# Kernel tuning notes

Measured on AMD Instinct MI355X. Metric: run time of the kernel, lower is better.

## Reference

```python
import jax, jax.numpy as jnp
import numpy as np

T = 256   # time steps
F = 64    # features per step
H = 32    # LSTM hidden size
FORGET_BIAS = 1.0  # TF LSTMCell default


def setup_inputs() -> dict:
    key = jax.random.key(0)
    k1, k2, k3 = jax.random.split(key, 3)
    B = 16384
    x = jax.random.normal(k1, (B, T * F), dtype=jnp.float32)
    W_lstm = jax.random.normal(k2, (F + H, 4 * H), dtype=jnp.float32) * 0.1
    b_lstm = jnp.zeros((4 * H,), dtype=jnp.float32)
    W_dense = jax.random.normal(k3, (H, 1), dtype=jnp.float32) * 0.1
    b_dense = jnp.zeros((1,), dtype=jnp.float32)
    return {"x": x, "W_lstm": W_lstm, "b_lstm": b_lstm,
            "W_dense": W_dense, "b_dense": b_dense}


def reference(x, W_lstm, b_lstm, W_dense, b_dense):
    B = x.shape[0]
    # [B, T*F] -> [T, B, F] for scan over time
    xs = x.reshape(B, T, F).transpose(1, 0, 2)

    def step(carry, x_t):
        c, h = carry
        # TF LSTMCell: concat([inputs, h]) @ kernel + bias, gate order i, j, f, o
        gates = jnp.concatenate([x_t, h], axis=-1) @ W_lstm + b_lstm
        i, j, f, o = jnp.split(gates, 4, axis=-1)
        c_new = c * jax.nn.sigmoid(f + FORGET_BIAS) + jax.nn.sigmoid(i) * jnp.tanh(j)
        h_new = jnp.tanh(c_new) * jax.nn.sigmoid(o)
        return (c_new, h_new), None

    c0 = jnp.zeros((B, H), dtype=x.dtype)
    h0 = jnp.zeros((B, H), dtype=x.dtype)
    (c_T, h_T), _ = jax.lax.scan(step, (c0, h0), xs)

    # dense(1) + ELU on the final hidden state, then flatten like predict()
    out = jax.nn.elu(h_T @ W_dense + b_dense)
    return out.reshape(-1)
```

## Files before the change

kernel.cpp:

```cpp
#include <hip/hip_runtime.h>
#include <stdint.h>

#define T_STEPS 256
#define F_IN 64
#define L2E 1.44269504f

typedef __bf16 bf16x8 __attribute__((ext_vector_type(8)));
typedef float f32x4 __attribute__((ext_vector_type(4)));
typedef uint32_t u32;
typedef uint32_t u32x2 __attribute__((ext_vector_type(2)));
typedef uint32_t u32x4 __attribute__((ext_vector_type(4)));

#define GLDS16(gp, lp)                                                         \
    __builtin_amdgcn_global_load_lds(                                          \
        (const __attribute__((address_space(1))) unsigned int*)(gp),           \
        (__attribute__((address_space(3))) unsigned int*)(lp), 16, 0, 0)

static __device__ __forceinline__ u32 pk2(float lo, float hi) {
    unsigned short a = __builtin_bit_cast(unsigned short, (__bf16)lo);
    unsigned short b = __builtin_bit_cast(unsigned short, (__bf16)hi);
    return (u32)a | ((u32)b << 16);
}

__global__ __launch_bounds__(128, 2)
void lstm_fused(const float* __restrict__ x,
                const float* __restrict__ Wl,
                const float* __restrict__ bl,
                const float* __restrict__ Wd,
                const float* __restrict__ bd,
                float* __restrict__ out)
{
    __shared__ __align__(16) float  xs[4][1024];
    __shared__ __align__(16) __bf16 hf[2][64][8];

    const int lane = threadIdx.x & 63;
    const int wid  = threadIdx.x >> 6;
    const int cl   = lane & 15;
    const int g4   = lane >> 4;
    const int rowBase = blockIdx.x * 16;

    bf16x8 wfrag[3][4];
#pragma unroll
    for (int kc = 0; kc < 3; ++kc) {
#pragma unroll
        for (int qi = 0; qi < 4; ++qi) {
            bf16x8 v;
#pragma unroll
            for (int j = 0; j < 8; ++j)
                v[j] = (__bf16)Wl[(kc * 32 + g4 * 8 + j) * 128 + (2 * qi + wid) * 16 + cl];
            wfrag[kc][qi] = v;
        }
    }

    float KI[4], KJ[4], KF[4], KO[4];
    {
        const int u0 = wid * 16 + g4 * 4;
#pragma unroll
        for (int r = 0; r < 4; ++r) {
            KI[r] = -L2E        *  bl[      u0 + r];
            KJ[r] = -2.0f * L2E *  bl[ 32 + u0 + r];
            KF[r] = -L2E        * (bl[ 64 + u0 + r] + 1.0f);
            KO[r] = -L2E        *  bl[ 96 + u0 + r];
        }
    }
    const float bd0 = bd[0];
    const f32x4 wdA = *(const f32x4*)(Wd + g4 * 8);
    const f32x4 wdB = *(const f32x4*)(Wd + g4 * 8 + 4);

    const float* gbase = x + (size_t)(rowBase + (lane >> 2)) * (size_t)(T_STEPS * F_IN)
                           + (size_t)(((lane & 3) ^ ((lane >> 3) & 3)) * 4);

    if (threadIdx.x < 64)
        *reinterpret_cast<u32x4*>(&hf[0][threadIdx.x][0]) = u32x4{0u, 0u, 0u, 0u};

    asm volatile("s_waitcnt vmcnt(0)" ::: "memory");
    __builtin_amdgcn_sched_barrier(0);

#pragma unroll
    for (int s = 0; s < 3; ++s) {
        const float* gp = gbase + s * F_IN + wid * 32;
        GLDS16(gp,      &xs[s][wid * 512]);
        GLDS16(gp + 16, &xs[s][wid * 512 + 256]);
    }

    asm volatile("s_waitcnt vmcnt(4) lgkmcnt(0)" ::: "memory");
    __builtin_amdgcn_sched_barrier(0);
    __builtin_amdgcn_s_barrier();
    __builtin_amdgcn_sched_barrier(0);

    const int swz = (cl >> 1) & 3;
    const int c0  = ((g4 & 1) * 2)     ^ swz;
    const int c1  = ((g4 & 1) * 2 + 1) ^ swz;
    const int kA  = (g4 >> 1) * 256 + cl * 16;
    const int kB  = kA + 512;
    const f32x4 z4 = {0.f, 0.f, 0.f, 0.f};

    const int tT = (2 * wid + (g4 >> 1)) * 16 + cl;
    const int e0 = (g4 & 1) * 4;

    float c_st[4] = {0.f, 0.f, 0.f, 0.f};

#define STEP(TT, SLOT) do {                                                    \
    const int par = (SLOT) & 1;                                                \
     \
    const float* sl = &xs[SLOT][0];                                            \
    f32x4 xr0 = *(const f32x4*)(sl + kA + c0 * 4);                             \
    f32x4 xr1 = *(const f32x4*)(sl + kA + c1 * 4);                             \
    f32x4 xr2 = *(const f32x4*)(sl + kB + c0 * 4);                             \
    f32x4 xr3 = *(const f32x4*)(sl + kB + c1 * 4);                             \
    bf16x8 ah = *reinterpret_cast<const bf16x8*>(&hf[par][lane][0]);           \
                                                   \
    const int tpf = ((TT) + 3 < T_STEPS) ? (TT) + 3 : T_STEPS - 1;             \
    const float* gp = gbase + tpf * F_IN + wid * 32;                           \
    GLDS16(gp,      &xs[((SLOT)+3)&3][wid * 512]);                             \
    GLDS16(gp + 16, &xs[((SLOT)+3)&3][wid * 512 + 256]);                       \
    bf16x8 ax0, ax1;                                                           \
    _Pragma("unroll")                                                          \
    for (int j = 0; j < 4; ++j) {                                              \
        ax0[j]     = (__bf16)xr0[j];                                           \
        ax0[4 + j] = (__bf16)xr1[j];                                           \
        ax1[j]     = (__bf16)xr2[j];                                           \
        ax1[4 + j] = (__bf16)xr3[j];                                           \
    }                                                                          \
    f32x4 acc[4];                                                              \
    __builtin_amdgcn_s_setprio(1);                                             \
    _Pragma("unroll")                                                          \
    for (int qi = 0; qi < 4; ++qi) {                                           \
        f32x4 a = __builtin_amdgcn_mfma_f32_16x16x32_bf16(wfrag[0][qi], ax0, z4, 0, 0, 0); \
        a = __builtin_amdgcn_mfma_f32_16x16x32_bf16(wfrag[1][qi], ax1, a, 0, 0, 0);        \
        a = __builtin_amdgcn_mfma_f32_16x16x32_bf16(wfrag[2][qi], ah,  a, 0, 0, 0);        \
        acc[qi] = a;                                                           \
    }                                                                          \
    __builtin_amdgcn_s_setprio(0);                                             \
    \
    float hh[4];                                                               \
    _Pragma("unroll")                                                          \
    for (int r = 0; r < 4; ++r) {                                              \
        float I  = __builtin_amdgcn_exp2f(__builtin_fmaf(acc[0][r], -L2E,        KI[r])); \
        float J  = __builtin_amdgcn_exp2f(__builtin_fmaf(acc[1][r], -2.0f * L2E, KJ[r])); \
        float P  = (1.0f - J) * __builtin_amdgcn_rcpf((1.0f + I) * (1.0f + J)); \
        float Fv = __builtin_amdgcn_exp2f(__builtin_fmaf(acc[2][r], -L2E,        KF[r])); \
        float S  = __builtin_amdgcn_rcpf(1.0f + Fv);                           \
        float cn = __builtin_fmaf(c_st[r], S, P);                              \
        float C  = __builtin_amdgcn_exp2f(-2.0f * L2E * cn);                   \
        float O  = __builtin_amdgcn_exp2f(__builtin_fmaf(acc[3][r], -L2E,      KO[r])); \
        hh[r] = (1.0f - C) * __builtin_amdgcn_rcpf((1.0f + C) * (1.0f + O));   \
        c_st[r] = cn;                                                          \
    }                                                                          \
    *reinterpret_cast<u32x2*>(&hf[par ^ 1][tT][e0]) =                          \
        u32x2{pk2(hh[0], hh[1]), pk2(hh[2], hh[3])};                           \
    asm volatile("s_waitcnt vmcnt(4) lgkmcnt(0)" ::: "memory");                \
    __builtin_amdgcn_sched_barrier(0);                                         \
    __builtin_amdgcn_s_barrier();                                              \
    __builtin_amdgcn_sched_barrier(0);                                         \
} while (0)

    for (int t = 0; t < T_STEPS; t += 4) {
        STEP(t,     0);
        STEP(t + 1, 1);
        STEP(t + 2, 2);
        STEP(t + 3, 3);
    }
#undef STEP

    if (wid == 0) {
        bf16x8 hfin = *reinterpret_cast<const bf16x8*>(&hf[0][lane][0]);
        float v = 0.f;
#pragma unroll
        for (int j = 0; j < 4; ++j) {
            v = __builtin_fmaf((float)hfin[j],     wdA[j], v);
            v = __builtin_fmaf((float)hfin[4 + j], wdB[j], v);
        }
        v += __shfl_xor(v, 16, 64);
        v += __shfl_xor(v, 32, 64);
        if (lane < 16) {
            float z = v + bd0;
            out[rowBase + lane] = z > 0.f ? z : (__expf(z) - 1.0f);
        }
    }
}

extern "C" void kernel_launch(void* const* d_in, const int* in_sizes, int n_in,
                              void* d_out, int out_size, void* d_ws, size_t ws_size,
                              hipStream_t stream) {
    const float* x  = (const float*)d_in[0];
    const float* Wl = (const float*)d_in[1];
    const float* bl = (const float*)d_in[2];
    const float* Wd = (const float*)d_in[3];
    const float* bd = (const float*)d_in[4];
    float* out = (float*)d_out;

    const int rows = out_size;
    const int grid = (rows + 15) / 16;
    hipLaunchKernelGGL(lstm_fused, dim3(grid), dim3(128), 0, stream,
                       x, Wl, bl, Wd, bd, out);
}
```

Before: 262.3 us.

## Batch x prefetch into 4-step stages with 8-slot LDS ring

Replaces per-step prefetch of one timestep into a 4-slot LDS ring with a batched prefetch of four timesteps every fourth step into an 8-slot ring. Each wave now loads whole 64-float rows for two timesteps instead of half rows for every step. The vmcnt wait is now needed only once per four steps, which removes per-step memory waits from the serial recurrence. In exchange LDS use doubles, which may reduce occupancy, and each issue burst is larger.

New measurement: 262.9 us. Within noise of the previous version (+0.2%).

```diff
diff --git a/kernel.cpp b/kernel.cpp
--- a/kernel.cpp
+++ b/kernel.cpp
@@ -30,7 +30,7 @@
                 const float* __restrict__ bd,
                 float* __restrict__ out)
 {
-    __shared__ __align__(16) float  xs[4][1024];
+    __shared__ __align__(16) float  xs[8][1024];
     __shared__ __align__(16) __bf16 hf[2][64][8];
 
     const int lane = threadIdx.x & 63;
@@ -76,14 +76,22 @@
     asm volatile("s_waitcnt vmcnt(0)" ::: "memory");
     __builtin_amdgcn_sched_barrier(0);
 
-#pragma unroll
-    for (int s = 0; s < 3; ++s) {
-        const float* gp = gbase + s * F_IN + wid * 32;
-        GLDS16(gp,      &xs[s][wid * 512]);
-        GLDS16(gp + 16, &xs[s][wid * 512 + 256]);
-    }
-
-    asm volatile("s_waitcnt vmcnt(4) lgkmcnt(0)" ::: "memory");
+#define STAGE(TB) do {                                                         \
+    _Pragma("unroll")                                                          \
+    for (int s2 = 0; s2 < 2; ++s2) {                                           \
+        const int st  = (TB) + 2 * wid + s2;                                   \
+        const int sl8 = st & 7;                                                \
+        const float* gp = gbase + st * F_IN;                                   \
+        GLDS16(gp,      &xs[sl8][0]);                                          \
+        GLDS16(gp + 16, &xs[sl8][256]);                                        \
+        GLDS16(gp + 32, &xs[sl8][512]);                                        \
+        GLDS16(gp + 48, &xs[sl8][768]);                                        \
+    }                                                                          \
+} while (0)
+
+    STAGE(0);
+    STAGE(4);
+    asm volatile("s_waitcnt vmcnt(8) lgkmcnt(0)" ::: "memory");
     __builtin_amdgcn_sched_barrier(0);
     __builtin_amdgcn_s_barrier();
     __builtin_amdgcn_sched_barrier(0);
@@ -100,20 +108,14 @@
 
     float c_st[4] = {0.f, 0.f, 0.f, 0.f};
 
-#define STEP(TT, SLOT) do {                                                    \
-    const int par = (SLOT) & 1;                                                \
-     \
-    const float* sl = &xs[SLOT][0];                                            \
+#define STEP(TT, PH) do {                                                      \
+    const int par = (TT) & 1;                                                  \
+    const float* sl = &xs[(TT) & 7][0];                                        \
     f32x4 xr0 = *(const f32x4*)(sl + kA + c0 * 4);                             \
     f32x4 xr1 = *(const f32x4*)(sl + kA + c1 * 4);                             \
     f32x4 xr2 = *(const f32x4*)(sl + kB + c0 * 4);                             \
     f32x4 xr3 = *(const f32x4*)(sl + kB + c1 * 4);                             \
     bf16x8 ah = *reinterpret_cast<const bf16x8*>(&hf[par][lane][0]);           \
-                                                   \
-    const int tpf = ((TT) + 3 < T_STEPS) ? (TT) + 3 : T_STEPS - 1;             \
-    const float* gp = gbase + tpf * F_IN + wid * 32;                           \
-    GLDS16(gp,      &xs[((SLOT)+3)&3][wid * 512]);                             \
-    GLDS16(gp + 16, &xs[((SLOT)+3)&3][wid * 512 + 256]);                       \
     bf16x8 ax0, ax1;                                                           \
     _Pragma("unroll")                                                          \
     for (int j = 0; j < 4; ++j) {                                              \
@@ -132,7 +134,6 @@
         acc[qi] = a;                                                           \
     }                                                                          \
     __builtin_amdgcn_s_setprio(0);                                             \
-    \
     float hh[4];                                                               \
     _Pragma("unroll")                                                          \
     for (int r = 0; r < 4; ++r) {                                              \
@@ -149,7 +150,16 @@
     }                                                                          \
     *reinterpret_cast<u32x2*>(&hf[par ^ 1][tT][e0]) =                          \
         u32x2{pk2(hh[0], hh[1]), pk2(hh[2], hh[3])};                           \
-    asm volatile("s_waitcnt vmcnt(4) lgkmcnt(0)" ::: "memory");                \
+    if ((PH) == 3) {                                                           \
+        if ((TT) + 5 < T_STEPS) {                                              \
+            STAGE((TT) + 5);                                                   \
+            asm volatile("s_waitcnt vmcnt(8) lgkmcnt(0)" ::: "memory");        \
+        } else {                                                               \
+            asm volatile("s_waitcnt vmcnt(0) lgkmcnt(0)" ::: "memory");        \
+        }                                                                      \
+    } else {                                                                   \
+        asm volatile("s_waitcnt lgkmcnt(0)" ::: "memory");                     \
+    }                                                                          \
     __builtin_amdgcn_sched_barrier(0);                                         \
     __builtin_amdgcn_s_barrier();                                              \
     __builtin_amdgcn_sched_barrier(0);                                         \
@@ -162,6 +172,7 @@
         STEP(t + 3, 3);
     }
 #undef STEP
+#undef STAGE
 
     if (wid == 0) {
         bf16x8 hfin = *reinterpret_cast<const bf16x8*>(&hf[0][lane][0]);
```

## Give each wave independent rows with two interleaved row groups, removing block barriers

Applied to the files above, without the earlier changes.

Instead of two waves splitting the gate columns of one 16-row tile and syncing through shared memory every step, each wave now owns 32 rows (two 16-row groups) and computes all 128 gate columns itself. This removes the per-step s_barrier, and the two independent recurrences are interleaved to hide MFMA and transcendental latency. Prefetch moves to a 3-slot per-wave ring staged two steps ahead. In exchange each wave keeps twice the weight fragments in registers, launch bounds drop to one block per SIMD pair, and the grid shrinks to a quarter as many blocks, so fewer waves may be resident to hide memory latency.

Result: slower. 401.9 us (+53.2%).

```diff
diff --git a/kernel.cpp b/kernel.cpp
--- a/kernel.cpp
+++ b/kernel.cpp
@@ -22,7 +22,7 @@
     return (u32)a | ((u32)b << 16);
 }
 
-__global__ __launch_bounds__(128, 2)
+__global__ __launch_bounds__(128, 1)
 void lstm_fused(const float* __restrict__ x,
                 const float* __restrict__ Wl,
                 const float* __restrict__ bl,
@@ -30,63 +30,69 @@
                 const float* __restrict__ bd,
                 float* __restrict__ out)
 {
-    __shared__ __align__(16) float  xs[4][1024];
-    __shared__ __align__(16) __bf16 hf[2][64][8];
+    __shared__ __align__(16) float  xs[2][3][2][1024];
+    __shared__ __align__(16) __bf16 hb[2][2][16][32];
 
     const int lane = threadIdx.x & 63;
     const int wid  = threadIdx.x >> 6;
     const int cl   = lane & 15;
     const int g4   = lane >> 4;
-    const int rowBase = blockIdx.x * 16;
-
-    bf16x8 wfrag[3][4];
+    const int rowBase = blockIdx.x * 64 + wid * 32;
+
+    bf16x8 wfrag[3][8];
 #pragma unroll
     for (int kc = 0; kc < 3; ++kc) {
 #pragma unroll
-        for (int qi = 0; qi < 4; ++qi) {
+        for (int qi = 0; qi < 8; ++qi) {
             bf16x8 v;
 #pragma unroll
             for (int j = 0; j < 8; ++j)
-                v[j] = (__bf16)Wl[(kc * 32 + g4 * 8 + j) * 128 + (2 * qi + wid) * 16 + cl];
+                v[j] = (__bf16)Wl[(kc * 32 + g4 * 8 + j) * 128 + qi * 16 + cl];
             wfrag[kc][qi] = v;
         }
     }
 
-    float KI[4], KJ[4], KF[4], KO[4];
-    {
-        const int u0 = wid * 16 + g4 * 4;
+    float KI[2][4], KJ[2][4], KF[2][4], KO[2][4];
+#pragma unroll
+    for (int uh = 0; uh < 2; ++uh) {
+        const int u0 = uh * 16 + g4 * 4;
 #pragma unroll
         for (int r = 0; r < 4; ++r) {
-            KI[r] = -L2E        *  bl[      u0 + r];
-            KJ[r] = -2.0f * L2E *  bl[ 32 + u0 + r];
-            KF[r] = -L2E        * (bl[ 64 + u0 + r] + 1.0f);
-            KO[r] = -L2E        *  bl[ 96 + u0 + r];
+            KI[uh][r] = -L2E        *  bl[      u0 + r];
+            KJ[uh][r] = -2.0f * L2E *  bl[ 32 + u0 + r];
+            KF[uh][r] = -L2E        * (bl[ 64 + u0 + r] + 1.0f);
+            KO[uh][r] = -L2E        *  bl[ 96 + u0 + r];
         }
     }
     const float bd0 = bd[0];
-    const f32x4 wdA = *(const f32x4*)(Wd + g4 * 8);
-    const f32x4 wdB = *(const f32x4*)(Wd + g4 * 8 + 4);
-
-    const float* gbase = x + (size_t)(rowBase + (lane >> 2)) * (size_t)(T_STEPS * F_IN)
-                           + (size_t)(((lane & 3) ^ ((lane >> 3) & 3)) * 4);
-
-    if (threadIdx.x < 64)
-        *reinterpret_cast<u32x4*>(&hf[0][threadIdx.x][0]) = u32x4{0u, 0u, 0u, 0u};
+    const f32x4 wd0 = *(const f32x4*)(Wd + g4 * 8);
+    const f32x4 wd1 = *(const f32x4*)(Wd + g4 * 8 + 4);
+
+    const float* gbA = x + (size_t)(rowBase + (lane >> 2)) * (size_t)(T_STEPS * F_IN)
+                         + (size_t)(((lane & 3) ^ ((lane >> 3) & 3)) * 4);
+    const float* gbB = gbA + (size_t)16 * (size_t)(T_STEPS * F_IN);
+
+    *reinterpret_cast<u32x4*>(&hb[wid][0][cl][g4 * 8]) = u32x4{0u, 0u, 0u, 0u};
+    *reinterpret_cast<u32x4*>(&hb[wid][1][cl][g4 * 8]) = u32x4{0u, 0u, 0u, 0u};
 
     asm volatile("s_waitcnt vmcnt(0)" ::: "memory");
     __builtin_amdgcn_sched_barrier(0);
 
-#pragma unroll
-    for (int s = 0; s < 3; ++s) {
-        const float* gp = gbase + s * F_IN + wid * 32;
-        GLDS16(gp,      &xs[s][wid * 512]);
-        GLDS16(gp + 16, &xs[s][wid * 512 + 256]);
-    }
-
-    asm volatile("s_waitcnt vmcnt(4) lgkmcnt(0)" ::: "memory");
-    __builtin_amdgcn_sched_barrier(0);
-    __builtin_amdgcn_s_barrier();
-    __builtin_amdgcn_sched_barrier(0);
+#define STAGE(TT, SP) do {                                                     \
+    const float* gpA = gbA + (TT) * F_IN;                                      \
+    GLDS16(gpA,      &xs[wid][SP][0][0]);                                      \
+    GLDS16(gpA + 16, &xs[wid][SP][0][256]);                                    \
+    GLDS16(gpA + 32, &xs[wid][SP][0][512]);                                    \
+    GLDS16(gpA + 48, &xs[wid][SP][0][768]);                                    \
+    const float* gpB = gbB + (TT) * F_IN;                                      \
+    GLDS16(gpB,      &xs[wid][SP][1][0]);                                      \
+    GLDS16(gpB + 16, &xs[wid][SP][1][256]);                                    \
+    GLDS16(gpB + 32, &xs[wid][SP][1][512]);                                    \
+    GLDS16(gpB + 48, &xs[wid][SP][1][768]);                                    \
+} while (0)
+
+    STAGE(0, 0);
+    STAGE(1, 1);
 
     const int swz = (cl >> 1) & 3;
     const int c0  = ((g4 & 1) * 2)     ^ swz;
@@ -95,25 +101,16 @@
     const int kB  = kA + 512;
     const f32x4 z4 = {0.f, 0.f, 0.f, 0.f};
 
-    const int tT = (2 * wid + (g4 >> 1)) * 16 + cl;
-    const int e0 = (g4 & 1) * 4;
-
-    float c_st[4] = {0.f, 0.f, 0.f, 0.f};
-
-#define STEP(TT, SLOT) do {                                                    \
-    const int par = (SLOT) & 1;                                                \
-     \
-    const float* sl = &xs[SLOT][0];                                            \
+    float csA[2][4] = {{0.f,0.f,0.f,0.f},{0.f,0.f,0.f,0.f}};
+    float csB[2][4] = {{0.f,0.f,0.f,0.f},{0.f,0.f,0.f,0.f}};
+
+#define TSTEP(G, SL, CS) do {                                                  \
+    const float* sl = &xs[wid][SL][G][0];                                      \
     f32x4 xr0 = *(const f32x4*)(sl + kA + c0 * 4);                             \
     f32x4 xr1 = *(const f32x4*)(sl + kA + c1 * 4);                             \
     f32x4 xr2 = *(const f32x4*)(sl + kB + c0 * 4);                             \
     f32x4 xr3 = *(const f32x4*)(sl + kB + c1 * 4);                             \
-    bf16x8 ah = *reinterpret_cast<const bf16x8*>(&hf[par][lane][0]);           \
-                                                   \
-    const int tpf = ((TT) + 3 < T_STEPS) ? (TT) + 3 : T_STEPS - 1;             \
-    const float* gp = gbase + tpf * F_IN + wid * 32;                           \
-    GLDS16(gp,      &xs[((SLOT)+3)&3][wid * 512]);                             \
-    GLDS16(gp + 16, &xs[((SLOT)+3)&3][wid * 512 + 256]);                       \
+    bf16x8 ah = *reinterpret_cast<const bf16x8*>(&hb[wid][G][cl][g4 * 8]);     \
     bf16x8 ax0, ax1;                                                           \
     _Pragma("unroll")                                                          \
     for (int j = 0; j < 4; ++j) {                                              \
@@ -122,60 +119,72 @@
         ax1[j]     = (__bf16)xr2[j];                                           \
         ax1[4 + j] = (__bf16)xr3[j];                                           \
     }                                                                          \
-    f32x4 acc[4];                                                              \
-    __builtin_amdgcn_s_setprio(1);                                             \
+    f32x4 acc[8];                                                              \
     _Pragma("unroll")                                                          \
-    for (int qi = 0; qi < 4; ++qi) {                                           \
+    for (int qi = 0; qi < 8; ++qi) {                                           \
         f32x4 a = __builtin_amdgcn_mfma_f32_16x16x32_bf16(wfrag[0][qi], ax0, z4, 0, 0, 0); \
         a = __builtin_amdgcn_mfma_f32_16x16x32_bf16(wfrag[1][qi], ax1, a, 0, 0, 0);        \
         a = __builtin_amdgcn_mfma_f32_16x16x32_bf16(wfrag[2][qi], ah,  a, 0, 0, 0);        \
         acc[qi] = a;                                                           \
     }                                                                          \
-    __builtin_amdgcn_s_setprio(0);                                             \
-    \
-    float hh[4];                                                               \
+    float hh[2][4];                                                            \
     _Pragma("unroll")                                                          \
-    for (int r = 0; r < 4; ++r) {                                              \
-        float I  = __builtin_amdgcn_exp2f(__builtin_fmaf(acc[0][r], -L2E,        KI[r])); \
-        float J  = __builtin_amdgcn_exp2f(__builtin_fmaf(acc[1][r], -2.0f * L2E, KJ[r])); \
-        float P  = (1.0f - J) * __builtin_amdgcn_rcpf((1.0f + I) * (1.0f + J)); \
-        float Fv = __builtin_amdgcn_exp2f(__builtin_fmaf(acc[2][r], -L2E,        KF[r])); \
-        float S  = __builtin_amdgcn_rcpf(1.0f + Fv);                           \
-        float cn = __builtin_fmaf(c_st[r], S, P);                              \
-        float C  = __builtin_amdgcn_exp2f(-2.0f * L2E * cn);                   \
-        float O  = __builtin_amdgcn_exp2f(__builtin_fmaf(acc[3][r], -L2E,      KO[r])); \
-        hh[r] = (1.0f - C) * __builtin_amdgcn_rcpf((1.0f + C) * (1.0f + O));   \
-        c_st[r] = cn;                                                          \
+    for (int uh = 0; uh < 2; ++uh) {                                           \
+        _Pragma("unroll")                                                      \
+        for (int r = 0; r < 4; ++r) {                                          \
+            float I  = __builtin_amdgcn_exp2f(__builtin_fmaf(acc[0+uh][r], -L2E,        KI[uh][r])); \
+            float J  = __builtin_amdgcn_exp2f(__builtin_fmaf(acc[2+uh][r], -2.0f * L2E, KJ[uh][r])); \
+            float P  = (1.0f - J) * __builtin_amdgcn_rcpf((1.0f + I) * (1.0f + J));      \
+            float Fv = __builtin_amdgcn_exp2f(__builtin_fmaf(acc[4+uh][r], -L2E,        KF[uh][r])); \
+            float S  = __builtin_amdgcn_rcpf(1.0f + Fv);                       \
+            float cn = __builtin_fmaf(CS[uh][r], S, P);                        \
+            float C  = __builtin_amdgcn_exp2f(-2.0f * L2E * cn);               \
+            float O  = __builtin_amdgcn_exp2f(__builtin_fmaf(acc[6+uh][r], -L2E, KO[uh][r])); \
+            hh[uh][r] = (1.0f - C) * __builtin_amdgcn_rcpf((1.0f + C) * (1.0f + O));     \
+            CS[uh][r] = cn;                                                    \
+        }                                                                      \
     }                                                                          \
-    *reinterpret_cast<u32x2*>(&hf[par ^ 1][tT][e0]) =                          \
-        u32x2{pk2(hh[0], hh[1]), pk2(hh[2], hh[3])};                           \
-    asm volatile("s_waitcnt vmcnt(4) lgkmcnt(0)" ::: "memory");                \
+    *reinterpret_cast<u32x2*>(&hb[wid][G][cl][g4 * 4]) =                       \
+        u32x2{pk2(hh[0][0], hh[0][1]), pk2(hh[0][2], hh[0][3])};               \
+    *reinterpret_cast<u32x2*>(&hb[wid][G][cl][16 + g4 * 4]) =                  \
+        u32x2{pk2(hh[1][0], hh[1][1]), pk2(hh[1][2], hh[1][3])};               \
+} while (0)
+
+#define ITER(TT, SL, SP, WN) do {                                              \
+    asm volatile("s_waitcnt vmcnt(" #WN ")" ::: "memory");                     \
     __builtin_amdgcn_sched_barrier(0);                                         \
-    __builtin_amdgcn_s_barrier();                                              \
-    __builtin_amdgcn_sched_barrier(0);                                         \
+    if ((TT) + 2 < T_STEPS) STAGE((TT) + 2, SP);                               \
+    TSTEP(0, SL, csA);                                                         \
+    TSTEP(1, SL, csB);                                                         \
 } while (0)
 
-    for (int t = 0; t < T_STEPS; t += 4) {
-        STEP(t,     0);
-        STEP(t + 1, 1);
-        STEP(t + 2, 2);
-        STEP(t + 3, 3);
-    }
-#undef STEP
-
-    if (wid == 0) {
-        bf16x8 hfin = *reinterpret_cast<const bf16x8*>(&hf[0][lane][0]);
+    for (int t = 0; t < 252; t += 3) {
+        ITER(t,     0, 2, 8);
+        ITER(t + 1, 1, 0, 8);
+        ITER(t + 2, 2, 1, 8);
+    }
+    ITER(252, 0, 2, 8);
+    ITER(253, 1, 0, 8);
+    ITER(254, 2, 1, 8);
+    ITER(255, 0, 2, 0);
+#undef ITER
+#undef TSTEP
+#undef STAGE
+
+#pragma unroll
+    for (int G = 0; G < 2; ++G) {
+        bf16x8 hfin = *reinterpret_cast<const bf16x8*>(&hb[wid][G][cl][g4 * 8]);
         float v = 0.f;
 #pragma unroll
         for (int j = 0; j < 4; ++j) {
-            v = __builtin_fmaf((float)hfin[j],     wdA[j], v);
-            v = __builtin_fmaf((float)hfin[4 + j], wdB[j], v);
+            v = __builtin_fmaf((float)hfin[j],     wd0[j], v);
+            v = __builtin_fmaf((float)hfin[4 + j], wd1[j], v);
         }
         v += __shfl_xor(v, 16, 64);
         v += __shfl_xor(v, 32, 64);
         if (lane < 16) {
             float z = v + bd0;
-            out[rowBase + lane] = z > 0.f ? z : (__expf(z) - 1.0f);
+            out[rowBase + G * 16 + lane] = z > 0.f ? z : (__expf(z) - 1.0f);
         }
     }
 }
@@ -191,7 +200,7 @@
     float* out = (float*)d_out;
 
     const int rows = out_size;
-    const int grid = (rows + 15) / 16;
+    const int grid = (rows + 63) / 64;
     hipLaunchKernelGGL(lstm_fused, dim3(grid), dim3(128), 0, stream,
                        x, Wl, bl, Wd, bd, out);
 }
```
